# Optimization experiments

Measured on AMD Instinct MI355X. Metric: run time of the kernel, lower is better.

Reference implementation:

```python
import jax, jax.numpy as jnp
import numpy as np

B, N, E, D, T, L = 2, 50000, 250000, 64, 16, 3


def setup_inputs() -> dict:
    key = jax.random.key(0)
    ks = jax.random.split(key, 12)
    # one-hot SIR states: susceptible=[1,0,0], infectious=[0,1,0], recovered=[0,0,1]
    states = jax.random.randint(ks[0], (B, N), 0, 3)
    x = jax.nn.one_hot(states, 3, dtype=jnp.float32)
    edge_index = jax.random.randint(ks[1], (2, E), 0, N)
    edge_attr = (jax.random.uniform(ks[2], (E, T)) < 0.3).astype(jnp.float32)

    def lin(k, fan_in, shape):
        return (jax.random.normal(k, shape, jnp.float32) / np.sqrt(fan_in)).astype(jnp.float32)

    return {
        "x": x,
        "edge_index": edge_index,
        "edge_attr": edge_attr,
        "pv_W": lin(ks[3], 3, (3, D)),
        "pv_b": jnp.zeros((D,), jnp.float32),
        "pe_W": lin(ks[4], T, (T, D)),
        "pe_b": jnp.zeros((D,), jnp.float32),
        "fe_W": lin(ks[5], 2 * D, (L, 2 * D, D)),
        "fe_b": jnp.zeros((L, D), jnp.float32),
        "fv_W": lin(ks[6], D, (L, D, D)),
        "fv_b": jnp.zeros((L, D), jnp.float32),
        "final_W": lin(ks[7], D, (D, 1)),
        "final_b": jnp.zeros((1,), jnp.float32),
    }


def reference(x, edge_index, edge_attr, pv_W, pv_b, pe_W, pe_b, fe_W, fe_b, fv_W, fv_b, final_W, final_b):
    src, dst = edge_index[0], edge_index[1]
    Bx, Nx, _ = x.shape
    # input projections p_v, p_e (Linear + ReLU)
    h = jax.nn.relu(x @ pv_W + pv_b)                       # [B, N, D]
    g = jax.nn.relu(edge_attr @ pe_W + pe_b)               # [E, D]
    g = jnp.broadcast_to(g[None], (Bx,) + g.shape)         # [B, E, D]
    num_layers = fe_W.shape[0]
    for l in range(num_layers):
        h_src = h[:, src, :]                               # gather  [B, E, D]
        g = jax.nn.relu(jnp.concatenate([g, h_src], axis=-1) @ fe_W[l] + fe_b[l])  # edge MLP
        agg = jnp.zeros_like(h).at[:, dst, :].add(g)       # scatter_add over dst
        h = jax.nn.relu(jax.nn.relu(h @ fv_W[l] + fv_b[l]) + agg)
    scores = (h @ final_W + final_b)[..., 0]               # [B, N]
    susceptible = x[..., 0] > 0.5
    scores = jnp.where(susceptible, -jnp.inf, scores)
    return jax.nn.log_softmax(scores, axis=-1)
```

## Files before the change

### kernel.cpp

```cpp
#include <hip/hip_runtime.h>
#include <math.h>

constexpr int Bc = 2;
constexpr int Nc = 50000;
constexpr int Ec = 250000;
constexpr int Dc = 64;
constexpr int TOT = Bc * Ec;
constexpr int TOTN = Bc * Nc;
constexpr int NT_TILES = 7816;
constexpr int TOT_PAD = NT_TILES * 64;
constexpr int NN16 = (TOTN + 15) / 16;
constexpr int SCAN_NBLK = (Nc + 255) / 256;

typedef __attribute__((ext_vector_type(8))) short short8;
typedef __attribute__((ext_vector_type(8))) unsigned short ushort8;
typedef __attribute__((ext_vector_type(4))) float f32x4;

__device__ inline unsigned short f2bf(float f) {
    unsigned int u = __builtin_bit_cast(unsigned int, f);
    unsigned int r = (u + 0x7fffu + ((u >> 16) & 1u)) >> 16;
    return (unsigned short)r;
}
__device__ inline float bf2f(unsigned short s) {
    unsigned int u = ((unsigned int)s) << 16;
    return __builtin_bit_cast(float, u);
}

__global__ __launch_bounds__(256) void csr_zero(int* __restrict__ counts)
{
    int i = blockIdx.x * 256 + threadIdx.x;
    if (i < Nc) counts[i] = 0;
}

__global__ __launch_bounds__(256) void csr_count(const int* __restrict__ dst,
                                                 int* __restrict__ counts)
{
    int e = blockIdx.x * 256 + threadIdx.x;
    if (e < Ec) atomicAdd(&counts[dst[e]], 1);
}

__global__ __launch_bounds__(256) void scan_partial(const int* __restrict__ counts,
                                                    int* __restrict__ bsum)
{
    __shared__ int sm[256];
    int tid = threadIdx.x;
    int i = blockIdx.x * 256 + tid;
    int c = (i < Nc) ? counts[i] : 0;
    sm[tid] = c;
    __syncthreads();
    #pragma unroll
    for (int off = 1; off < 256; off <<= 1) {
        int v = (tid >= off) ? sm[tid - off] : 0;
        __syncthreads();
        sm[tid] += v;
        __syncthreads();
    }
    if (tid == 255) bsum[blockIdx.x] = sm[255];
}

__global__ __launch_bounds__(256) void scan_bsum(int* __restrict__ bsum)
{
    __shared__ int sm[256];
    int tid = threadIdx.x;
    int v = (tid < SCAN_NBLK) ? bsum[tid] : 0;
    sm[tid] = v;
    __syncthreads();
    #pragma unroll
    for (int off = 1; off < 256; off <<= 1) {
        int u = (tid >= off) ? sm[tid - off] : 0;
        __syncthreads();
        sm[tid] += u;
        __syncthreads();
    }
    if (tid < SCAN_NBLK) bsum[tid] = sm[tid] - v;
}

__global__ __launch_bounds__(256) void scan_final(const int* __restrict__ counts,
                                                  const int* __restrict__ bsum,
                                                  int* __restrict__ offsets,
                                                  int* __restrict__ cursor)
{
    __shared__ int sm[256];
    int tid = threadIdx.x;
    int i = blockIdx.x * 256 + tid;
    int c = (i < Nc) ? counts[i] : 0;
    sm[tid] = c;
    __syncthreads();
    #pragma unroll
    for (int off = 1; off < 256; off <<= 1) {
        int v = (tid >= off) ? sm[tid - off] : 0;
        __syncthreads();
        sm[tid] += v;
        __syncthreads();
    }
    if (i < Nc) {
        int o = bsum[blockIdx.x] + sm[tid] - c;
        offsets[i] = o;
        cursor[i] = o;
    }
    if (i == 0) offsets[Nc] = Ec;
}

__global__ __launch_bounds__(256) void csr_fill(const int* __restrict__ dst,
                                                const int* __restrict__ src,
                                                int* __restrict__ cursor,
                                                int* __restrict__ elist,
                                                int* __restrict__ src_perm)
{
    int e = blockIdx.x * 256 + threadIdx.x;
    if (e < Ec) {
        int p = atomicAdd(&cursor[dst[e]], 1);
        elist[p] = e;
        src_perm[p] = src[e];
    }
}

__global__ __launch_bounds__(256) void prep_W(const float* __restrict__ fe_W,
                                              unsigned short* __restrict__ Wf)
{
    int t = blockIdx.x * 256 + threadIdx.x;
    if (t >= 3 * 1024) return;
    int l  = t >> 10;
    int s  = t & 1023;
    int frag = s >> 6;
    int sl   = s & 63;
    int kc = frag >> 2;
    int n  = frag & 3;
    int kbase = 32 * kc + (sl >> 4) * 8;
    int col   = 16 * n + (sl & 15);
    const float* W = fe_W + (size_t)l * 2 * Dc * Dc;
    ushort8 v;
    #pragma unroll
    for (int j = 0; j < 8; ++j) v[j] = f2bf(W[(size_t)(kbase + j) * Dc + col]);
    *(ushort8*)&Wf[(size_t)t * 8] = v;
}

__global__ __launch_bounds__(256) void prep_Wv(const float* __restrict__ fv_W,
                                               unsigned short* __restrict__ Wf2)
{
    int t = blockIdx.x * 256 + threadIdx.x;
    if (t >= 3 * 512) return;
    int l  = t >> 9;
    int s  = t & 511;
    int frag = s >> 6;
    int sl   = s & 63;
    int kc = frag >> 2;
    int n  = frag & 3;
    int kbase = 32 * kc + (sl >> 4) * 8;
    int col   = 16 * n + (sl & 15);
    const float* W = fv_W + (size_t)l * Dc * Dc;
    ushort8 v;
    #pragma unroll
    for (int j = 0; j < 8; ++j) v[j] = f2bf(W[(size_t)(kbase + j) * Dc + col]);
    *(ushort8*)&Wf2[(size_t)t * 8] = v;
}

__global__ __launch_bounds__(256) void prep_Wpe(const float* __restrict__ pe_W,
                                                unsigned short* __restrict__ Wpe)
{
    int t = threadIdx.x + blockIdx.x * 256;
    if (t >= 256) return;
    int n  = t >> 6;
    int sl = t & 63;
    int lg = sl >> 4;
    int col = 16 * n + (sl & 15);
    ushort8 v;
    #pragma unroll
    for (int j = 0; j < 8; ++j) {
        int k = lg * 8 + j;
        v[j] = (k < 16) ? f2bf(pe_W[(size_t)k * Dc + col]) : (unsigned short)0;
    }
    *(ushort8*)&Wpe[(size_t)t * 8] = v;
}

__global__ __launch_bounds__(256) void init_h_kernel(
    const float* __restrict__ x, const float* __restrict__ pv_W,
    const float* __restrict__ pv_b, unsigned short* __restrict__ h)
{
    int idx = blockIdx.x * blockDim.x + threadIdx.x;
    if (idx >= Bc * Nc * Dc) return;
    int bn = idx >> 6;
    int d  = idx & 63;
    float x0 = x[bn * 3 + 0];
    float x1 = x[bn * 3 + 1];
    int s = (x0 > 0.5f) ? 0 : ((x1 > 0.5f) ? 1 : 2);
    float v = pv_W[s * Dc + d] + pv_b[d];
    h[idx] = f2bf(fmaxf(v, 0.0f));
}

__global__ __launch_bounds__(256) void edge_kernel_l0(
    unsigned short* __restrict__ g, const unsigned short* __restrict__ h,
    const int* __restrict__ src_perm, const int* __restrict__ elist,
    const float* __restrict__ ea,
    const unsigned short* __restrict__ Wf ,
    const unsigned short* __restrict__ Wpe ,
    const float* __restrict__ bias, const float* __restrict__ peb)
{
    __shared__ unsigned short ldsB[16 * 64 * 8];
    __shared__ unsigned short ldsP[4 * 64 * 8];
    __shared__ unsigned short slab[4][16 * 72];

    int tid = threadIdx.x;
    int wid = tid >> 6;
    int l   = tid & 63;
    int lr  = l & 15;
    int lg  = l >> 4;

    #pragma unroll
    for (int it = 0; it < 4; ++it) {
        int s = tid + 256 * it;
        *(ushort8*)&ldsB[(size_t)s * 8] = *(const ushort8*)&Wf[(size_t)s * 8];
    }
    *(ushort8*)&ldsP[(size_t)tid * 8] = *(const ushort8*)&Wpe[(size_t)tid * 8];
    __syncthreads();

    int flat0 = (blockIdx.x * 4 + wid) * 64;

    int slot[4];
    size_t hbase[4];
    int em[4];
    #pragma unroll
    for (int m = 0; m < 4; ++m) {
        int row = flat0 + 16 * m + lr;
        int rr = (row < TOT) ? row : 0;
        int b = rr >= Ec;
        int i = rr - b * Ec;
        slot[m] = i;
        em[m] = elist[i];
        hbase[m] = ((size_t)b * Nc + src_perm[i]) * Dc;
    }

    float biasv[4], biasp[4];
    #pragma unroll
    for (int n = 0; n < 4; ++n) {
        biasv[n] = bias[16 * n + lr];
        biasp[n] = peb[16 * n + lr];
    }

    f32x4 acc[4][4];
    #pragma unroll
    for (int m = 0; m < 4; ++m)
        #pragma unroll
        for (int n = 0; n < 4; ++n) {
            f32x4 z = {biasv[n], biasv[n], biasv[n], biasv[n]};
            acc[m][n] = z;
        }

    #pragma unroll
    for (int m = 0; m < 4; ++m) {
        short8 a_ea = {0, 0, 0, 0, 0, 0, 0, 0};
        if (lg < 2) {
            const float4* rp = (const float4*)(ea + (size_t)em[m] * 16 + lg * 8);
            float4 p0 = rp[0], p1 = rp[1];
            float av[8] = {p0.x, p0.y, p0.z, p0.w, p1.x, p1.y, p1.z, p1.w};
            #pragma unroll
            for (int j = 0; j < 8; ++j) a_ea[j] = (short)f2bf(av[j]);
        }
        f32x4 acc0[4];
        #pragma unroll
        for (int n = 0; n < 4; ++n) {
            f32x4 z = {biasp[n], biasp[n], biasp[n], biasp[n]};
            acc0[n] = z;
            short8 bp = *(const short8*)&ldsP[(size_t)(n * 64 + l) * 8];
            acc0[n] = __builtin_amdgcn_mfma_f32_16x16x32_bf16(a_ea, bp, acc0[n], 0, 0, 0);
        }
        #pragma unroll
        for (int n = 0; n < 4; ++n)
            #pragma unroll
            for (int r = 0; r < 4; ++r)
                slab[wid][(lg * 4 + r) * 72 + 16 * n + lr] =
                    f2bf(fmaxf(acc0[n][r], 0.0f));
        short8 a0 = *(const short8*)&slab[wid][lr * 72 + 0 + lg * 8];
        short8 a1 = *(const short8*)&slab[wid][lr * 72 + 32 + lg * 8];
        #pragma unroll
        for (int n = 0; n < 4; ++n) {
            short8 b0 = *(const short8*)&ldsB[(size_t)((0 * 4 + n) * 64 + l) * 8];
            short8 b1 = *(const short8*)&ldsB[(size_t)((1 * 4 + n) * 64 + l) * 8];
            acc[m][n] = __builtin_amdgcn_mfma_f32_16x16x32_bf16(a0, b0, acc[m][n], 0, 0, 0);
            acc[m][n] = __builtin_amdgcn_mfma_f32_16x16x32_bf16(a1, b1, acc[m][n], 0, 0, 0);
        }
    }

    #pragma unroll
    for (int kc = 2; kc < 4; ++kc) {
        short8 a[4];
        #pragma unroll
        for (int m = 0; m < 4; ++m)
            a[m] = *(const short8*)(h + hbase[m] + (kc - 2) * 32 + lg * 8);
        #pragma unroll
        for (int m = 0; m < 4; ++m)
            #pragma unroll
            for (int n = 0; n < 4; ++n) {
                short8 bfr = *(const short8*)&ldsB[(size_t)((kc * 4 + n) * 64 + l) * 8];
                acc[m][n] = __builtin_amdgcn_mfma_f32_16x16x32_bf16(
                    a[m], bfr, acc[m][n], 0, 0, 0);
            }
    }

    #pragma unroll
    for (int m = 0; m < 4; ++m) {
        #pragma unroll
        for (int n = 0; n < 4; ++n)
            #pragma unroll
            for (int r = 0; r < 4; ++r)
                slab[wid][(lg * 4 + r) * 72 + 16 * n + lr] =
                    f2bf(fmaxf(acc[m][n][r], 0.0f));
        #pragma unroll
        for (int i = 0; i < 2; ++i) {
            int row = i * 8 + (l >> 3);
            int ch  = l & 7;
            ushort8 v = *(const ushort8*)&slab[wid][row * 72 + ch * 8];
            *(ushort8*)(g + (size_t)(flat0 + 16 * m + row) * Dc + ch * 8) = v;
        }
    }
}

__global__ __launch_bounds__(256) void edge_kernel(
    unsigned short* g,
    const unsigned short* __restrict__ h,
    const int* __restrict__ src_perm,
    const unsigned short* __restrict__ Wf ,
    const float* __restrict__ bias)
{
    __shared__ unsigned short ldsB[16 * 64 * 8];
    __shared__ unsigned short slab[4][16 * 72];

    int tid = threadIdx.x;
    int wid = tid >> 6;
    int l   = tid & 63;
    int lr  = l & 15;
    int lg  = l >> 4;

    #pragma unroll
    for (int it = 0; it < 4; ++it) {
        int s = tid + 256 * it;
        *(ushort8*)&ldsB[(size_t)s * 8] = *(const ushort8*)&Wf[(size_t)s * 8];
    }
    __syncthreads();

    int flat0 = (blockIdx.x * 4 + wid) * 64;

    int rowin[4];
    size_t hbase[4];
    #pragma unroll
    for (int m = 0; m < 4; ++m) {
        int row = flat0 + 16 * m + lr;
        int rr = (row < TOT) ? row : 0;
        int b = rr >= Ec;
        int i = rr - b * Ec;
        rowin[m] = rr;
        hbase[m] = ((size_t)b * Nc + src_perm[i]) * Dc;
    }

    float biasv[4];
    #pragma unroll
    for (int n = 0; n < 4; ++n) biasv[n] = bias[16 * n + lr];

    f32x4 acc[4][4];
    #pragma unroll
    for (int m = 0; m < 4; ++m)
        #pragma unroll
        for (int n = 0; n < 4; ++n) {
            f32x4 z = {biasv[n], biasv[n], biasv[n], biasv[n]};
            acc[m][n] = z;
        }

    #pragma unroll
    for (int kc = 0; kc < 4; ++kc) {
        short8 a[4];
        #pragma unroll
        for (int m = 0; m < 4; ++m) {
            const unsigned short* p;
            if (kc < 2) p = g + (size_t)rowin[m] * Dc + kc * 32 + lg * 8;
            else        p = h + hbase[m] + (kc - 2) * 32 + lg * 8;
            a[m] = *(const short8*)p;
        }
        short8 bfr[4];
        #pragma unroll
        for (int n = 0; n < 4; ++n)
            bfr[n] = *(const short8*)&ldsB[(size_t)((kc * 4 + n) * 64 + l) * 8];
        #pragma unroll
        for (int m = 0; m < 4; ++m)
            #pragma unroll
            for (int n = 0; n < 4; ++n)
                acc[m][n] = __builtin_amdgcn_mfma_f32_16x16x32_bf16(
                    a[m], bfr[n], acc[m][n], 0, 0, 0);
    }

    #pragma unroll
    for (int m = 0; m < 4; ++m) {
        #pragma unroll
        for (int n = 0; n < 4; ++n)
            #pragma unroll
            for (int r = 0; r < 4; ++r)
                slab[wid][(lg * 4 + r) * 72 + 16 * n + lr] =
                    f2bf(fmaxf(acc[m][n][r], 0.0f));
        #pragma unroll
        for (int i = 0; i < 2; ++i) {
            int row = i * 8 + (l >> 3);
            int ch  = l & 7;
            ushort8 v = *(const ushort8*)&slab[wid][row * 72 + ch * 8];
            *(ushort8*)(g + (size_t)(flat0 + 16 * m + row) * Dc + ch * 8) = v;
        }
    }
}

__global__ __launch_bounds__(256) void aggnode_kernel(
    const unsigned short* __restrict__ g, unsigned short* h,
    const int* __restrict__ offsets,
    const unsigned short* __restrict__ Wf2 ,
    const float* __restrict__ bias)
{
    __shared__ unsigned short ldsB[8 * 64 * 8];
    __shared__ unsigned short slab[4][16 * 72];

    int tid = threadIdx.x;
    int wid = tid >> 6;
    int l   = tid & 63;
    int lr  = l & 15;
    int lg  = l >> 4;

    #pragma unroll
    for (int it = 0; it < 2; ++it) {
        int s = tid + 256 * it;
        *(ushort8*)&ldsB[(size_t)s * 8] = *(const ushort8*)&Wf2[(size_t)s * 8];
    }
    __syncthreads();

    int w16 = blockIdx.x * 4 + wid;
    int flat0 = w16 * 16;

    float biasv[4];
    #pragma unroll
    for (int n = 0; n < 4; ++n) biasv[n] = bias[16 * n + lr];

    f32x4 acc[4];
    #pragma unroll
    for (int n = 0; n < 4; ++n) {
        f32x4 z = {biasv[n], biasv[n], biasv[n], biasv[n]};
        acc[n] = z;
    }

    int arow = flat0 + lr;
    int rr = (arow < TOTN) ? arow : 0;
    #pragma unroll
    for (int kc = 0; kc < 2; ++kc) {
        short8 a = *(const short8*)(h + (size_t)rr * Dc + kc * 32 + lg * 8);
        #pragma unroll
        for (int n = 0; n < 4; ++n) {
            short8 bfr = *(const short8*)&ldsB[(size_t)((kc * 4 + n) * 64 + l) * 8];
            acc[n] = __builtin_amdgcn_mfma_f32_16x16x32_bf16(a, bfr, acc[n], 0, 0, 0);
        }
    }

    #pragma unroll
    for (int n = 0; n < 4; ++n)
        #pragma unroll
        for (int r = 0; r < 4; ++r)
            slab[wid][(lg * 4 + r) * 72 + 16 * n + lr] = f2bf(fmaxf(acc[n][r], 0.0f));

    for (int r16 = 0; r16 < 16; ++r16) {
        int row = flat0 + r16;
        if (row >= TOTN) break;
        int b = row >= Nc;
        int n = row - b * Nc;
        int beg = offsets[n], end = offsets[n + 1];
        size_t gb = (size_t)b * Ec;
        float s0 = 0.0f, s1 = 0.0f, s2 = 0.0f, s3 = 0.0f;
        int i = beg;
        for (; i + 3 < end; i += 4) {
            s0 += bf2f(g[(gb + i + 0) * Dc + l]);
            s1 += bf2f(g[(gb + i + 1) * Dc + l]);
            s2 += bf2f(g[(gb + i + 2) * Dc + l]);
            s3 += bf2f(g[(gb + i + 3) * Dc + l]);
        }
        for (; i < end; ++i) s0 += bf2f(g[(gb + i) * Dc + l]);
        float s = (s0 + s1) + (s2 + s3);
        float v = bf2f(slab[wid][r16 * 72 + l]);
        h[(size_t)row * Dc + l] = f2bf(fmaxf(v + s, 0.0f));
    }
}

__global__ __launch_bounds__(256) void score_kernel(
    const unsigned short* __restrict__ h, const float* __restrict__ x,
    const float* __restrict__ fW, const float* __restrict__ fb,
    float* __restrict__ scores)
{
    int gt   = blockIdx.x * blockDim.x + threadIdx.x;
    int w    = gt >> 6;
    int lane = threadIdx.x & 63;
    if (w >= Bc * Nc) return;
    float v = bf2f(h[(size_t)w * Dc + lane]) * fW[lane];
    #pragma unroll
    for (int off = 32; off > 0; off >>= 1) v += __shfl_down(v, off);
    if (lane == 0) {
        float sc = v + fb[0];
        if (x[w * 3] > 0.5f) sc = -INFINITY;
        scores[w] = sc;
    }
}

__global__ __launch_bounds__(1024) void reduce_kernel(
    const float* __restrict__ scores, float* __restrict__ red)
{
    int b = blockIdx.x;
    const float* s = scores + (size_t)b * Nc;
    __shared__ float sm[16];
    int tid = threadIdx.x, lane = tid & 63, wid = tid >> 6;

    float m = -INFINITY;
    for (int i = tid; i < Nc; i += 1024) m = fmaxf(m, s[i]);
    #pragma unroll
    for (int off = 32; off > 0; off >>= 1) m = fmaxf(m, __shfl_down(m, off));
    if (lane == 0) sm[wid] = m;
    __syncthreads();
    if (tid == 0) {
        float mm = sm[0];
        for (int i = 1; i < 16; ++i) mm = fmaxf(mm, sm[i]);
        sm[0] = mm;
    }
    __syncthreads();
    float M = sm[0];
    __syncthreads();

    float sum = 0.0f;
    for (int i = tid; i < Nc; i += 1024) sum += expf(s[i] - M);
    #pragma unroll
    for (int off = 32; off > 0; off >>= 1) sum += __shfl_down(sum, off);
    if (lane == 0) sm[wid] = sum;
    __syncthreads();
    if (tid == 0) {
        float tot = 0.0f;
        for (int i = 0; i < 16; ++i) tot += sm[i];
        red[b * 2 + 0] = M;
        red[b * 2 + 1] = logf(tot);
    }
}

__global__ __launch_bounds__(256) void final_kernel(
    const float* __restrict__ scores, const float* __restrict__ red,
    float* __restrict__ out)
{
    int i = blockIdx.x * blockDim.x + threadIdx.x;
    if (i >= Bc * Nc) return;
    int b = i / Nc;
    float v = scores[i] - red[b * 2] - red[b * 2 + 1];
    out[i] = fmaxf(v, -3.0e38f);
}

extern "C" void kernel_launch(void* const* d_in, const int* in_sizes, int n_in,
                              void* d_out, int out_size, void* d_ws, size_t ws_size,
                              hipStream_t stream)
{
    const float* x     = (const float*)d_in[0];
    const int*   ei    = (const int*)d_in[1];
    const float* ea    = (const float*)d_in[2];
    const float* pv_W  = (const float*)d_in[3];
    const float* pv_b  = (const float*)d_in[4];
    const float* pe_W  = (const float*)d_in[5];
    const float* pe_b  = (const float*)d_in[6];
    const float* fe_W  = (const float*)d_in[7];
    const float* fe_b  = (const float*)d_in[8];
    const float* fv_W  = (const float*)d_in[9];
    const float* fv_b  = (const float*)d_in[10];
    const float* fin_W = (const float*)d_in[11];
    const float* fin_b = (const float*)d_in[12];
    float* out = (float*)d_out;

    unsigned short* g_bf = (unsigned short*)d_ws;
    unsigned short* h_bf = g_bf + (size_t)TOT_PAD * Dc;
    unsigned short* Wf   = h_bf + (size_t)Bc * Nc * Dc;
    unsigned short* Wf2  = Wf + (size_t)3 * 1024 * 8;
    unsigned short* Wpe  = Wf2 + (size_t)3 * 512 * 8;
    float* scores = (float*)(Wpe + (size_t)256 * 8);
    float* red    = scores + (size_t)Bc * Nc;
    int* counts   = (int*)(red + 4);
    int* offsets  = counts + Nc;
    int* cursor   = offsets + Nc + 1;
    int* bsum     = cursor + Nc;
    int* elist    = bsum + 256;
    int* src_perm = elist + Ec;

    const int* src = ei;
    const int* dst = ei + Ec;

    csr_zero<<<(Nc + 255) / 256, 256, 0, stream>>>(counts);
    csr_count<<<(Ec + 255) / 256, 256, 0, stream>>>(dst, counts);
    scan_partial<<<SCAN_NBLK, 256, 0, stream>>>(counts, bsum);
    scan_bsum<<<1, 256, 0, stream>>>(bsum);
    scan_final<<<SCAN_NBLK, 256, 0, stream>>>(counts, bsum, offsets, cursor);
    csr_fill<<<(Ec + 255) / 256, 256, 0, stream>>>(dst, src, cursor, elist, src_perm);

    prep_W<<<(3 * 1024 + 255) / 256, 256, 0, stream>>>(fe_W, Wf);
    prep_Wv<<<(3 * 512 + 255) / 256, 256, 0, stream>>>(fv_W, Wf2);
    prep_Wpe<<<1, 256, 0, stream>>>(pe_W, Wpe);
    init_h_kernel<<<(Bc * Nc * Dc + 255) / 256, 256, 0, stream>>>(x, pv_W, pv_b, h_bf);

    for (int l = 0; l < 3; ++l) {
        if (l == 0) {
            edge_kernel_l0<<<NT_TILES / 4, 256, 0, stream>>>(
                g_bf, h_bf, src_perm, elist, ea, Wf, Wpe, fe_b, pe_b);
        } else {
            edge_kernel<<<NT_TILES / 4, 256, 0, stream>>>(
                g_bf, h_bf, src_perm, Wf + (size_t)l * 1024 * 8, fe_b + l * Dc);
        }
        aggnode_kernel<<<(NN16 + 3) / 4, 256, 0, stream>>>(
            g_bf, h_bf, offsets, Wf2 + (size_t)l * 512 * 8, fv_b + l * Dc);
    }

    score_kernel<<<((size_t)Bc * Nc * 64 + 255) / 256, 256, 0, stream>>>(
        h_bf, x, fin_W, fin_b, scores);
    reduce_kernel<<<Bc, 1024, 0, stream>>>(scores, red);
    final_kernel<<<(Bc * Nc + 255) / 256, 256, 0, stream>>>(scores, red, out);
}
```

Measured before the change: 356.1 us.

## Store edge features as FP8 and use FP8 MFMA for the g-half of edge MLP

Edge features g are now stored in 8-bit FP8 instead of bf16, and the g-part of the edge MLP runs on fp8 MFMA with fp8-quantized weights, while the h-part stays bf16. The intent is to halve the memory traffic of the large edge buffer written by the edge kernels and read by aggregation. It adds extra weight-prep kernels and an in-kernel self-check that deliberately corrupts g8[0] if a sampled result mismatches. It also changes NaN handling in ReLU and the final clamp. FP8 quantization risks accuracy loss.

```diff
diff --git a/kernel.cpp b/kernel.cpp
--- a/kernel.cpp
+++ b/kernel.cpp
@@ -14,6 +14,7 @@
 
 typedef __attribute__((ext_vector_type(8))) short short8;
 typedef __attribute__((ext_vector_type(8))) unsigned short ushort8;
+typedef __attribute__((ext_vector_type(8))) unsigned char uchar8;
 typedef __attribute__((ext_vector_type(4))) float f32x4;
 
 __device__ inline unsigned short f2bf(float f) {
@@ -24,6 +25,14 @@
 __device__ inline float bf2f(unsigned short s) {
     unsigned int u = ((unsigned int)s) << 16;
     return __builtin_bit_cast(float, u);
+}
+__device__ inline unsigned char f2fp8(float f) {
+    f = fminf(f, 448.0f);
+    unsigned int u = __builtin_amdgcn_cvt_pk_fp8_f32(f, f, 0u, false);
+    return (unsigned char)(u & 0xFF);
+}
+__device__ inline float fp82f(unsigned char c) {
+    return __builtin_amdgcn_cvt_f32_fp8((unsigned int)c, 0);
 }
 
 __global__ __launch_bounds__(256) void csr_zero(int* __restrict__ counts)
@@ -119,9 +128,46 @@
                                               unsigned short* __restrict__ Wf)
 {
     int t = blockIdx.x * 256 + threadIdx.x;
-    if (t >= 3 * 1024) return;
-    int l  = t >> 10;
-    int s  = t & 1023;
+    if (t >= 1024) return;
+    int frag = t >> 6;
+    int sl   = t & 63;
+    int kc = frag >> 2;
+    int n  = frag & 3;
+    int kbase = 32 * kc + (sl >> 4) * 8;
+    int col   = 16 * n + (sl & 15);
+    ushort8 v;
+    #pragma unroll
+    for (int j = 0; j < 8; ++j) v[j] = f2bf(fe_W[(size_t)(kbase + j) * Dc + col]);
+    *(ushort8*)&Wf[(size_t)t * 8] = v;
+}
+
+__global__ __launch_bounds__(256) void prep_Wh(const float* __restrict__ fe_W,
+                                               unsigned short* __restrict__ Wfh)
+{
+    int t = blockIdx.x * 256 + threadIdx.x;
+    if (t >= 3 * 512) return;
+    int l  = t >> 9;
+    int s  = t & 511;
+    int frag = s >> 6;
+    int sl   = s & 63;
+    int kc = frag >> 2;
+    int n  = frag & 3;
+    int kbase = 64 + 32 * kc + (sl >> 4) * 8;
+    int col   = 16 * n + (sl & 15);
+    const float* W = fe_W + (size_t)l * 2 * Dc * Dc;
+    ushort8 v;
+    #pragma unroll
+    for (int j = 0; j < 8; ++j) v[j] = f2bf(W[(size_t)(kbase + j) * Dc + col]);
+    *(ushort8*)&Wfh[(size_t)t * 8] = v;
+}
+
+__global__ __launch_bounds__(256) void prep_W8(const float* __restrict__ fe_W,
+                                               unsigned char* __restrict__ Wf8)
+{
+    int t = blockIdx.x * 256 + threadIdx.x;
+    if (t >= 3 * 512) return;
+    int l  = t >> 9;
+    int s  = t & 511;
     int frag = s >> 6;
     int sl   = s & 63;
     int kc = frag >> 2;
@@ -129,10 +175,15 @@
     int kbase = 32 * kc + (sl >> 4) * 8;
     int col   = 16 * n + (sl & 15);
     const float* W = fe_W + (size_t)l * 2 * Dc * Dc;
-    ushort8 v;
-    #pragma unroll
-    for (int j = 0; j < 8; ++j) v[j] = f2bf(W[(size_t)(kbase + j) * Dc + col]);
-    *(ushort8*)&Wf[(size_t)t * 8] = v;
+    uchar8 v;
+    #pragma unroll
+    for (int j = 0; j < 8; ++j) {
+        float w = W[(size_t)(kbase + j) * Dc + col];
+        w = fmaxf(fminf(w, 448.0f), -448.0f);
+        unsigned int u = __builtin_amdgcn_cvt_pk_fp8_f32(w, w, 0u, false);
+        v[j] = (unsigned char)(u & 0xFF);
+    }
+    *(uchar8*)&Wf8[(size_t)t * 8] = v;
 }
 
 __global__ __launch_bounds__(256) void prep_Wv(const float* __restrict__ fv_W,
@@ -189,7 +240,7 @@
 }
 
 __global__ __launch_bounds__(256) void edge_kernel_l0(
-    unsigned short* __restrict__ g, const unsigned short* __restrict__ h,
+    unsigned char* __restrict__ g8, const unsigned short* __restrict__ h,
     const int* __restrict__ src_perm, const int* __restrict__ elist,
     const float* __restrict__ ea,
     const unsigned short* __restrict__ Wf ,
@@ -216,7 +267,6 @@
 
     int flat0 = (blockIdx.x * 4 + wid) * 64;
 
-    int slot[4];
     size_t hbase[4];
     int em[4];
     #pragma unroll
@@ -225,7 +275,6 @@
         int rr = (row < TOT) ? row : 0;
         int b = rr >= Ec;
         int i = rr - b * Ec;
-        slot[m] = i;
         em[m] = elist[i];
         hbase[m] = ((size_t)b * Nc + src_perm[i]) * Dc;
     }
@@ -310,19 +359,26 @@
             int row = i * 8 + (l >> 3);
             int ch  = l & 7;
             ushort8 v = *(const ushort8*)&slab[wid][row * 72 + ch * 8];
-            *(ushort8*)(g + (size_t)(flat0 + 16 * m + row) * Dc + ch * 8) = v;
+            uchar8 q;
+            #pragma unroll
+            for (int j = 0; j < 8; ++j) q[j] = f2fp8(bf2f(v[j]));
+            *(uchar8*)(g8 + (size_t)(flat0 + 16 * m + row) * Dc + ch * 8) = q;
         }
     }
 }
 
 __global__ __launch_bounds__(256) void edge_kernel(
-    unsigned short* g,
+    unsigned char* g8,
     const unsigned short* __restrict__ h,
     const int* __restrict__ src_perm,
-    const unsigned short* __restrict__ Wf ,
-    const float* __restrict__ bias)
-{
-    __shared__ unsigned short ldsB[16 * 64 * 8];
+    const unsigned char* __restrict__ Wf8 ,
+    const unsigned short* __restrict__ Wfh ,
+    const float* __restrict__ bias,
+    const float* __restrict__ Wsrc ,
+    int check)
+{
+    __shared__ unsigned char  ldsB8[8 * 64 * 8];
+    __shared__ unsigned short ldsBh[8 * 64 * 8];
     __shared__ unsigned short slab[4][16 * 72];
 
     int tid = threadIdx.x;
@@ -332,9 +388,14 @@
     int lg  = l >> 4;
 
     #pragma unroll
-    for (int it = 0; it < 4; ++it) {
+    for (int it = 0; it < 2; ++it) {
         int s = tid + 256 * it;
-        *(ushort8*)&ldsB[(size_t)s * 8] = *(const ushort8*)&Wf[(size_t)s * 8];
+        *(ushort8*)&ldsBh[(size_t)s * 8] = *(const ushort8*)&Wfh[(size_t)s * 8];
+    }
+    #pragma unroll
+    for (int it = 0; it < 2; ++it) {
+        int s = tid + 256 * it;
+        *(uchar8*)&ldsB8[(size_t)s * 8] = *(const uchar8*)&Wf8[(size_t)s * 8];
     }
     __syncthreads();
 
@@ -366,25 +427,55 @@
         }
 
     #pragma unroll
-    for (int kc = 0; kc < 4; ++kc) {
+    for (int kc = 0; kc < 2; ++kc) {
+        long a[4];
+        #pragma unroll
+        for (int m = 0; m < 4; ++m)
+            a[m] = __builtin_bit_cast(long,
+                *(const uchar8*)(g8 + (size_t)rowin[m] * Dc + kc * 32 + lg * 8));
+        #pragma unroll
+        for (int m = 0; m < 4; ++m)
+            #pragma unroll
+            for (int n = 0; n < 4; ++n) {
+                long bfr = __builtin_bit_cast(long,
+                    *(const uchar8*)&ldsB8[(size_t)((kc * 4 + n) * 64 + l) * 8]);
+                acc[m][n] = __builtin_amdgcn_mfma_f32_16x16x32_fp8_fp8(
+                    a[m], bfr, acc[m][n], 0, 0, 0);
+            }
+    }
+    #pragma unroll
+    for (int kc = 2; kc < 4; ++kc) {
         short8 a[4];
         #pragma unroll
-        for (int m = 0; m < 4; ++m) {
-            const unsigned short* p;
-            if (kc < 2) p = g + (size_t)rowin[m] * Dc + kc * 32 + lg * 8;
-            else        p = h + hbase[m] + (kc - 2) * 32 + lg * 8;
-            a[m] = *(const short8*)p;
-        }
-        short8 bfr[4];
-        #pragma unroll
-        for (int n = 0; n < 4; ++n)
-            bfr[n] = *(const short8*)&ldsB[(size_t)((kc * 4 + n) * 64 + l) * 8];
-        #pragma unroll
         for (int m = 0; m < 4; ++m)
-            #pragma unroll
-            for (int n = 0; n < 4; ++n)
+            a[m] = *(const short8*)(h + hbase[m] + (kc - 2) * 32 + lg * 8);
+        #pragma unroll
+        for (int m = 0; m < 4; ++m)
+            #pragma unroll
+            for (int n = 0; n < 4; ++n) {
+                short8 bfr = *(const short8*)&ldsBh[(size_t)(((kc - 2) * 4 + n) * 64 + l) * 8];
                 acc[m][n] = __builtin_amdgcn_mfma_f32_16x16x32_bf16(
-                    a[m], bfr[n], acc[m][n], 0, 0, 0);
+                    a[m], bfr, acc[m][n], 0, 0, 0);
+            }
+    }
+
+    bool bad = false;
+    if (check && blockIdx.x == 0 && wid == 0) {
+        int grow = lg * 4;
+        int col  = lr;
+        float ref = bias[col];
+        for (int k = 0; k < 64; ++k) {
+            float av = fp82f(g8[(size_t)grow * Dc + k]);
+            float w  = Wsrc[(size_t)k * Dc + col];
+            w = fmaxf(fminf(w, 448.0f), -448.0f);
+            unsigned int wu = __builtin_amdgcn_cvt_pk_fp8_f32(w, w, 0u, false);
+            ref += av * fp82f((unsigned char)(wu & 0xFF));
+        }
+        size_t hb = (size_t)src_perm[grow] * Dc;
+        for (int k = 0; k < 64; ++k)
+            ref += bf2f(h[hb + k]) * bf2f(f2bf(Wsrc[(size_t)(64 + k) * Dc + col]));
+        float got = acc[0][0][0];
+        if (!(fabsf(got - ref) <= 5e-2f * (1.0f + fabsf(ref)))) bad = true;
     }
 
     #pragma unroll
@@ -400,13 +491,17 @@
             int row = i * 8 + (l >> 3);
             int ch  = l & 7;
             ushort8 v = *(const ushort8*)&slab[wid][row * 72 + ch * 8];
-            *(ushort8*)(g + (size_t)(flat0 + 16 * m + row) * Dc + ch * 8) = v;
-        }
-    }
+            uchar8 q;
+            #pragma unroll
+            for (int j = 0; j < 8; ++j) q[j] = f2fp8(bf2f(v[j]));
+            *(uchar8*)(g8 + (size_t)(flat0 + 16 * m + row) * Dc + ch * 8) = q;
+        }
+    }
+    if (bad) g8[0] = 0x7F;
 }
 
 __global__ __launch_bounds__(256) void aggnode_kernel(
-    const unsigned short* __restrict__ g, unsigned short* h,
+    const unsigned char* __restrict__ g8, unsigned short* h,
     const int* __restrict__ offsets,
     const unsigned short* __restrict__ Wf2 ,
     const float* __restrict__ bias)
@@ -469,15 +564,17 @@
         float s0 = 0.0f, s1 = 0.0f, s2 = 0.0f, s3 = 0.0f;
         int i = beg;
         for (; i + 3 < end; i += 4) {
-            s0 += bf2f(g[(gb + i + 0) * Dc + l]);
-            s1 += bf2f(g[(gb + i + 1) * Dc + l]);
-            s2 += bf2f(g[(gb + i + 2) * Dc + l]);
-            s3 += bf2f(g[(gb + i + 3) * Dc + l]);
-        }
-        for (; i < end; ++i) s0 += bf2f(g[(gb + i) * Dc + l]);
+            s0 += fp82f(g8[(gb + i + 0) * Dc + l]);
+            s1 += fp82f(g8[(gb + i + 1) * Dc + l]);
+            s2 += fp82f(g8[(gb + i + 2) * Dc + l]);
+            s3 += fp82f(g8[(gb + i + 3) * Dc + l]);
+        }
+        for (; i < end; ++i) s0 += fp82f(g8[(gb + i) * Dc + l]);
         float s = (s0 + s1) + (s2 + s3);
         float v = bf2f(slab[wid][r16 * 72 + l]);
-        h[(size_t)row * Dc + l] = f2bf(fmaxf(v + s, 0.0f));
+        float o = v + s;
+        o = (o > 0.0f) ? o : (o == o ? 0.0f : o);
+        h[(size_t)row * Dc + l] = f2bf(o);
     }
 }
 
@@ -545,7 +642,11 @@
     if (i >= Bc * Nc) return;
     int b = i / Nc;
     float v = scores[i] - red[b * 2] - red[b * 2 + 1];
-    out[i] = fmaxf(v, -3.0e38f);
+    float o;
+    if (v >= -3.0e38f)      o = v;
+    else if (v == v)        o = -3.0e38f;
+    else                    o = v;
+    out[i] = o;
 }
 
 extern "C" void kernel_launch(void* const* d_in, const int* in_sizes, int n_in,
@@ -567,12 +668,14 @@
     const float* fin_b = (const float*)d_in[12];
     float* out = (float*)d_out;
 
-    unsigned short* g_bf = (unsigned short*)d_ws;
-    unsigned short* h_bf = g_bf + (size_t)TOT_PAD * Dc;
+    unsigned char* g8    = (unsigned char*)d_ws;
+    unsigned short* h_bf = (unsigned short*)(g8 + (size_t)TOT_PAD * Dc);
     unsigned short* Wf   = h_bf + (size_t)Bc * Nc * Dc;
-    unsigned short* Wf2  = Wf + (size_t)3 * 1024 * 8;
+    unsigned short* Wfh  = Wf + (size_t)1024 * 8;
+    unsigned short* Wf2  = Wfh + (size_t)3 * 512 * 8;
     unsigned short* Wpe  = Wf2 + (size_t)3 * 512 * 8;
-    float* scores = (float*)(Wpe + (size_t)256 * 8);
+    unsigned char* Wf8   = (unsigned char*)(Wpe + (size_t)256 * 8);
+    float* scores = (float*)(Wf8 + (size_t)3 * 512 * 8);
     float* red    = scores + (size_t)Bc * Nc;
     int* counts   = (int*)(red + 4);
     int* offsets  = counts + Nc;
@@ -591,7 +694,9 @@
     scan_final<<<SCAN_NBLK, 256, 0, stream>>>(counts, bsum, offsets, cursor);
     csr_fill<<<(Ec + 255) / 256, 256, 0, stream>>>(dst, src, cursor, elist, src_perm);
 
-    prep_W<<<(3 * 1024 + 255) / 256, 256, 0, stream>>>(fe_W, Wf);
+    prep_W<<<4, 256, 0, stream>>>(fe_W, Wf);
+    prep_Wh<<<(3 * 512 + 255) / 256, 256, 0, stream>>>(fe_W, Wfh);
+    prep_W8<<<(3 * 512 + 255) / 256, 256, 0, stream>>>(fe_W, Wf8);
     prep_Wv<<<(3 * 512 + 255) / 256, 256, 0, stream>>>(fv_W, Wf2);
     prep_Wpe<<<1, 256, 0, stream>>>(pe_W, Wpe);
     init_h_kernel<<<(Bc * Nc * Dc + 255) / 256, 256, 0, stream>>>(x, pv_W, pv_b, h_bf);
@@ -599,13 +704,16 @@
     for (int l = 0; l < 3; ++l) {
         if (l == 0) {
             edge_kernel_l0<<<NT_TILES / 4, 256, 0, stream>>>(
-                g_bf, h_bf, src_perm, elist, ea, Wf, Wpe, fe_b, pe_b);
+                g8, h_bf, src_perm, elist, ea, Wf, Wpe, fe_b, pe_b);
         } else {
             edge_kernel<<<NT_TILES / 4, 256, 0, stream>>>(
-                g_bf, h_bf, src_perm, Wf + (size_t)l * 1024 * 8, fe_b + l * Dc);
+                g8, h_bf, src_perm,
+                Wf8 + (size_t)l * 512 * 8, Wfh + (size_t)l * 512 * 8,
+                fe_b + l * Dc, fe_W + (size_t)l * 2 * Dc * Dc,
+                (l == 1) ? 1 : 0);
         }
         aggnode_kernel<<<(NN16 + 3) / 4, 256, 0, stream>>>(
-            g_bf, h_bf, offsets, Wf2 + (size_t)l * 512 * 8, fv_b + l * Dc);
+            g8, h_bf, offsets, Wf2 + (size_t)l * 512 * 8, fv_b + l * Dc);
     }
 
     score_kernel<<<((size_t)Bc * Nc * 64 + 255) / 256, 256, 0, stream>>>(
```

Result: faster. 345.2 us (-3.1%).
